# Kernel tuning notes

Measured on AMD Instinct MI355X. Metric: run time of the kernel, lower is better.

The kernel has to match this reference:

```python
import jax, jax.numpy as jnp
import numpy as np

# Qwen3.5 GatedDeltaNet dims
B, T, HID = 2, 2048, 2048
HK, HV, DK, DV, KW = 16, 32, 128, 128, 4   # k-heads, v-heads, head dims, conv kernel
R = HV // HK                                # GQA repeat factor = 2
KEY_DIM = HK * DK                           # 2048
VAL_DIM = HV * DV                           # 4096
CONV_DIM = 2 * KEY_DIM + VAL_DIM            # 8192
EPS = 1e-6


def setup_inputs() -> dict:
    key = jax.random.key(0)
    ks = jax.random.split(key, 10)
    w = lambda k, shape, s=0.02: (jax.random.normal(k, shape) * s).astype(jnp.float32)
    A = jax.random.uniform(ks[8], (HV,), minval=1e-3, maxval=16.0)
    return {
        "hidden_states": jax.random.normal(ks[0], (B, T, HID), jnp.float32),
        "W_qkv": w(ks[1], (HID, CONV_DIM)),
        "W_z": w(ks[2], (HID, VAL_DIM)),
        "W_b": w(ks[3], (HID, HV)),
        "W_a": w(ks[4], (HID, HV)),
        "conv_w": w(ks[5], (CONV_DIM, KW), 0.5),   # depthwise causal conv taps
        "dt_bias": jnp.ones((HV,), jnp.float32),
        "A_log": jnp.log(A).astype(jnp.float32),
        "norm_weight": jnp.ones((DV,), jnp.float32),
        "W_out": w(ks[9], (VAL_DIM, HID)),
    }


def _forward(hidden_states, W_qkv, W_z, W_b, W_a, conv_w, dt_bias, A_log, norm_weight, W_out):
    x = hidden_states
    # --- projections ---
    qkv = x @ W_qkv                                    # [B,T,CONV_DIM]
    z = x @ W_z                                        # [B,T,VAL_DIM]
    beta = jax.nn.sigmoid(x @ W_b)                     # [B,T,HV]
    alpha = x @ W_a                                    # [B,T,HV]
    g = -jnp.exp(A_log) * jax.nn.softplus(alpha + dt_bias)  # [B,T,HV] (log-decay <= 0)

    # --- fix_query_key_value_ordering: per-k-head interleaved layout ---
    qkv = qkv.reshape(B, T, HK, 2 * DK + R * DV)
    q, k, v = jnp.split(qkv, [DK, 2 * DK], axis=3)
    mixed = jnp.concatenate([q.reshape(B, T, -1), k.reshape(B, T, -1), v.reshape(B, T, -1)], axis=-1)

    # --- causal depthwise short conv (kernel 4) + SiLU ---
    xp = jnp.pad(mixed, ((0, 0), (KW - 1, 0), (0, 0)))
    conv = sum(conv_w[:, i] * xp[:, i:i + T, :] for i in range(KW))
    conv = jax.nn.silu(conv)

    q, k, v = jnp.split(conv, [KEY_DIM, 2 * KEY_DIM], axis=-1)
    q = q.reshape(B, T, HK, DK)
    k = k.reshape(B, T, HK, DK)
    v = v.reshape(B, T, HV, DV)
    gate = z.reshape(B, T, HV, DV)

    # GQA: repeat q,k heads to match v heads
    q = jnp.repeat(q, R, axis=2)                       # [B,T,HV,DK]
    k = jnp.repeat(k, R, axis=2)

    # l2-norm q,k (use_qk_l2norm_in_kernel=True) and default scale 1/sqrt(DK)
    q = q / jnp.sqrt(jnp.sum(q * q, axis=-1, keepdims=True) + 1e-6)
    k = k / jnp.sqrt(jnp.sum(k * k, axis=-1, keepdims=True) + 1e-6)
    q = q * (DK ** -0.5)

    # --- gated delta rule recurrence (scan over time) ---
    # state S: [B,HV,DK,DV];  S_t = a_t*S_{t-1} + k_t (beta_t*(v_t - (a_t*S_{t-1})^T k_t))^T
    def step(S, inp):
        qt, kt, vt, gt, bt = inp                       # [B,HV,DK],[B,HV,DK],[B,HV,DV],[B,HV],[B,HV]
        S = S * jnp.exp(gt)[:, :, None, None]
        kv = jnp.einsum('bhk,bhkv->bhv', kt, S)
        delta = bt[..., None] * (vt - kv)              # [B,HV,DV]
        S = S + kt[..., None] * delta[:, :, None, :]
        o = jnp.einsum('bhk,bhkv->bhv', qt, S)
        return S, o

    tfirst = lambda a: jnp.moveaxis(a, 1, 0)           # [T,B,...]
    S0 = jnp.zeros((B, HV, DK, DV), q.dtype)
    _, o = jax.lax.scan(step, S0, (tfirst(q), tfirst(k), tfirst(v), tfirst(g), tfirst(beta)))
    o = jnp.moveaxis(o, 0, 1)                          # [B,T,HV,DV]

    # --- gated RMSNorm: rmsnorm(o) * silu(gate) * weight ---
    var = jnp.mean(o * o, axis=-1, keepdims=True)
    o = o * jax.lax.rsqrt(var + EPS)
    o = o * jax.nn.silu(gate)
    o = o * norm_weight

    return o.reshape(B, T, VAL_DIM) @ W_out            # [B,T,HID]


def reference(hidden_states, W_qkv, W_z, W_b, W_a, conv_w, dt_bias, A_log, norm_weight, W_out):
    return _forward(hidden_states, W_qkv, W_z, W_b, W_a, conv_w, dt_bias, A_log, norm_weight, W_out)
```

## Files before the change

kernel.cpp:

```cpp
#include <hip/hip_runtime.h>


#define T_LEN 2048
#define MROWS 4096

typedef __bf16 bf16x8 __attribute__((ext_vector_type(8)));
typedef float f32x4 __attribute__((ext_vector_type(4)));

#define MFMA(a, b, c) __builtin_amdgcn_mfma_f32_16x16x32_bf16((a), (b), (c), 0, 0, 0)

__device__ __forceinline__ unsigned short f2bf(float f) {
  unsigned int u = __float_as_uint(f);
  unsigned int r = (u + 0x7fffu + ((u >> 16) & 1u)) >> 16;
  return (unsigned short)r;
}
__device__ __forceinline__ float bf2f(unsigned short u) {
  return __uint_as_float(((unsigned int)u) << 16);
}
__device__ __forceinline__ void gload_lds16(const void* g, void* l) {
  __builtin_amdgcn_global_load_lds(
      (const __attribute__((address_space(1))) unsigned int*)g,
      (__attribute__((address_space(3))) unsigned int*)l, 16, 0, 0);
}

__global__ __launch_bounds__(256) void f32_to_bf16_vec(const float* __restrict__ src,
                                                       unsigned short* __restrict__ dst,
                                                       int n4) {
  int i = blockIdx.x * 256 + threadIdx.x;
  if (i >= n4) return;
  float4 v = ((const float4*)src)[i];
  ushort4 o;
  o.x = f2bf(v.x); o.y = f2bf(v.y); o.z = f2bf(v.z); o.w = f2bf(v.w);
  ((ushort4*)dst)[i] = o;
}

__global__ __launch_bounds__(256) void transpose_f2b(const float* __restrict__ src,
                                                     unsigned short* __restrict__ dst,
                                                     int R, int C) {
  __shared__ float tile[32][33];
  int tx = threadIdx.x & 31, ty = threadIdx.x >> 5;
  int c0 = blockIdx.x * 32, r0 = blockIdx.y * 32;
  #pragma unroll
  for (int i = ty; i < 32; i += 8)
    tile[i][tx] = src[(size_t)(r0 + i) * C + c0 + tx];
  __syncthreads();
  #pragma unroll
  for (int i = ty; i < 32; i += 8)
    dst[(size_t)(c0 + i) * R + r0 + tx] = f2bf(tile[tx][i]);
}

template <int OUTBF>
__global__ __launch_bounds__(512, 2) void gemm8p(const unsigned short* __restrict__ A, int lda,
                                                 const unsigned short* __restrict__ Bt, int ldb,
                                                 void* __restrict__ Cv, int ldc,
                                                 int M, int N, int K) {
  __shared__ unsigned short lds[65536];

  const int mtiles = M >> 8;
  const int nwg = gridDim.x, orig = blockIdx.x;
  const int q = nwg >> 3, r = nwg & 7;
  const int xcd = orig & 7, idx = orig >> 3;
  const int swz = (xcd < r ? xcd * (q + 1) : r * (q + 1) + (xcd - r) * q) + idx;
  const int m0 = (swz % mtiles) * 256;
  const int n0 = (swz / mtiles) * 256;

  const int tid = threadIdx.x, lane = tid & 63, wv = tid >> 6;
  const int wm = wv >> 2, wn = wv & 3;
  const int l15 = lane & 15, l4 = lane >> 4;

  f32x4 acc[8][4];
  #pragma unroll
  for (int i = 0; i < 8; i++)
    #pragma unroll
    for (int j = 0; j < 4; j++) acc[i][j] = f32x4{0.f, 0.f, 0.f, 0.f};

  const int NT = K >> 6;

  auto SHALF = [&](int t, int op, int h) {
    unsigned short* base = lds + (t & 1) * 32768 + op * 16384 + h * 8192;
    const unsigned short* G = op ? Bt : A;
    const int ld = op ? ldb : lda;
    const int r0g = (op ? n0 : m0) + h * 128;
    const int k0 = t << 6;
    #pragma unroll
    for (int is = 0; is < 2; is++) {
      int ow = is * 8192 + wv * 1024;
      int o = ow + lane * 16;
      int row = o >> 7, colB = o & 127;
      int scol = colB ^ ((row & 7) << 4);
      gload_lds16(G + (size_t)(r0g + row) * ld + k0 + (scol >> 1), base + (ow >> 1));
    }
  };

  bf16x8 aF[4][2], bF[2][2];
  auto RD_A = [&](int t, int qm) {
    const unsigned short* base = lds + (t & 1) * 32768 + qm * 8192;
    #pragma unroll
    for (int mi = 0; mi < 4; mi++) {
      int ra = wm * 64 + mi * 16 + l15;
      int sw = (ra & 7) << 4;
      #pragma unroll
      for (int kh = 0; kh < 2; kh++) {
        int colB = kh * 64 + l4 * 16;
        aF[mi][kh] = *(const bf16x8*)(base + ra * 64 + ((colB ^ sw) >> 1));
      }
    }
  };
  auto RD_B = [&](int t, int qn) {
    const unsigned short* base = lds + (t & 1) * 32768 + 16384 + qn * 8192;
    #pragma unroll
    for (int ni = 0; ni < 2; ni++) {
      int rb = wn * 32 + ni * 16 + l15;
      int sw = (rb & 7) << 4;
      #pragma unroll
      for (int kh = 0; kh < 2; kh++) {
        int colB = kh * 64 + l4 * 16;
        bF[ni][kh] = *(const bf16x8*)(base + rb * 64 + ((colB ^ sw) >> 1));
      }
    }
  };
  auto COMPUTE = [&](int qm, int qn) {
    __builtin_amdgcn_s_setprio(1);
    #pragma unroll
    for (int mi = 0; mi < 4; mi++)
      #pragma unroll
      for (int ni = 0; ni < 2; ni++)
        #pragma unroll
        for (int kh = 0; kh < 2; kh++)
          acc[qm * 4 + mi][qn * 2 + ni] =
              MFMA(aF[mi][kh], bF[ni][kh], acc[qm * 4 + mi][qn * 2 + ni]);
    __builtin_amdgcn_s_setprio(0);
  };
  auto SBAR = [&]() {
    __builtin_amdgcn_sched_barrier(0);
    __builtin_amdgcn_s_barrier();
    __builtin_amdgcn_sched_barrier(0);
  };

  SHALF(0, 0, 0); SHALF(0, 1, 0); SHALF(0, 1, 1); SHALF(0, 0, 1);
  asm volatile("s_waitcnt vmcnt(4)" ::: "memory");
  SBAR();

  for (int t = 0; t < NT; t++) {
    const bool lastT = (t + 1 >= NT);
    RD_A(t, 0); RD_B(t, 0);
    if (!lastT) SHALF(t + 1, 0, 0);
    COMPUTE(0, 0);
    if (!lastT) asm volatile("s_waitcnt vmcnt(4)" ::: "memory");
    else        asm volatile("s_waitcnt vmcnt(2)" ::: "memory");
    SBAR();
    RD_B(t, 1);
    if (!lastT) SHALF(t + 1, 1, 0);
    COMPUTE(0, 1);
    if (!lastT) asm volatile("s_waitcnt vmcnt(4)" ::: "memory");
    else        asm volatile("s_waitcnt vmcnt(0)" ::: "memory");
    SBAR();
    RD_A(t, 1);
    if (!lastT) SHALF(t + 1, 1, 1);
    COMPUTE(1, 1);
    RD_B(t, 0);
    if (!lastT) SHALF(t + 1, 0, 1);
    COMPUTE(1, 0);
    if (!lastT) {
      asm volatile("s_waitcnt vmcnt(4)" ::: "memory");
      SBAR();
    }
  }

  #pragma unroll
  for (int i = 0; i < 8; i++) {
    int grow = m0 + (i >> 2) * 128 + wm * 64 + (i & 3) * 16 + l4 * 4;
    #pragma unroll
    for (int j = 0; j < 4; j++) {
      int gcol = n0 + (j >> 1) * 128 + wn * 32 + (j & 1) * 16 + l15;
      if (OUTBF) {
        unsigned short* cp = (unsigned short*)Cv + (size_t)grow * ldc + gcol;
        #pragma unroll
        for (int rr = 0; rr < 4; rr++) cp[(size_t)rr * ldc] = f2bf(acc[i][j][rr]);
      } else {
        float* cp = (float*)Cv + (size_t)grow * ldc + gcol;
        #pragma unroll
        for (int rr = 0; rr < 4; rr++) cp[(size_t)rr * ldc] = acc[i][j][rr];
      }
    }
  }
}

template <int OUTBF, int BN>
__global__ __launch_bounds__(512, 2) void gemm256(const unsigned short* __restrict__ A, int lda,
                                                  const unsigned short* __restrict__ Bt, int ldb,
                                                  void* __restrict__ Cv, int ldc,
                                                  int M, int N, int K) {
  constexpr int BUFSZ = 16384 + BN * 64;
  constexpr int BISS = BN / 64;
  constexpr int IS = 4 + BISS;
  constexpr int WMv = (BN == 256) ? 2 : 4;
  constexpr int MSUB = 256 / (WMv * 16);
  constexpr int MSPAN = 256 / WMv;

  __shared__ unsigned short lds[2 * BUFSZ];

  const int mtiles = M >> 8;
  const int nwg = gridDim.x;
  const int orig = blockIdx.x;
  const int q = nwg >> 3, r = nwg & 7;
  const int xcd = orig & 7, idx = orig >> 3;
  const int swz = (xcd < r ? xcd * (q + 1) : r * (q + 1) + (xcd - r) * q) + idx;
  const int m0 = (swz % mtiles) * 256;
  const int n0 = (swz / mtiles) * BN;

  const int tid = threadIdx.x, lane = tid & 63, wv = tid >> 6;
  const int wm = (BN == 256) ? (wv >> 2) : (wv >> 1);
  const int wn = (BN == 256) ? (wv & 3) : (wv & 1);
  const int l15 = lane & 15, l4 = lane >> 4;

  f32x4 acc[MSUB][4];
  #pragma unroll
  for (int i = 0; i < MSUB; i++)
    #pragma unroll
    for (int j = 0; j < 4; j++) acc[i][j] = f32x4{0.f, 0.f, 0.f, 0.f};

  const int NT = K >> 6;

  auto STAGE = [&](int kt) {
    unsigned short* base = lds + (kt & 1) * BUFSZ;
    const int k0 = kt << 6;
    #pragma unroll
    for (int is = 0; is < 4; is++) {
      int ow = is * 8192 + wv * 1024;
      int o = ow + lane * 16;
      int row = o >> 7, colB = o & 127;
      int scol = colB ^ ((row & 7) << 4);
      gload_lds16(A + (size_t)(m0 + row) * lda + k0 + (scol >> 1), base + (ow >> 1));
    }
    #pragma unroll
    for (int is = 0; is < BISS; is++) {
      int ow = is * 8192 + wv * 1024;
      int o = ow + lane * 16;
      int row = o >> 7, colB = o & 127;
      int scol = colB ^ ((row & 7) << 4);
      gload_lds16(Bt + (size_t)(n0 + row) * ldb + k0 + (scol >> 1), base + 16384 + (ow >> 1));
    }
  };

  STAGE(0);
  if (NT > 1) STAGE(1);
  if constexpr (IS == 8) asm volatile("s_waitcnt vmcnt(8)" ::: "memory");
  else                   asm volatile("s_waitcnt vmcnt(6)" ::: "memory");
  __builtin_amdgcn_sched_barrier(0);
  __builtin_amdgcn_s_barrier();
  __builtin_amdgcn_sched_barrier(0);

  for (int t = 0; t < NT; t++) {
    const unsigned short* Abuf = lds + (t & 1) * BUFSZ;
    const unsigned short* Bbuf = Abuf + 16384;
    bf16x8 bF[4][2];
    #pragma unroll
    for (int n = 0; n < 4; n++) {
      int rb = wn * 64 + n * 16 + l15;
      int sw = (rb & 7) << 4;
      #pragma unroll
      for (int ks = 0; ks < 2; ks++) {
        int colB = (ks * 32 + l4 * 8) * 2;
        bF[n][ks] = *(const bf16x8*)(Bbuf + rb * 64 + ((colB ^ sw) >> 1));
      }
    }
    __builtin_amdgcn_s_setprio(1);
    #pragma unroll
    for (int m = 0; m < MSUB; m++) {
      int ra = wm * MSPAN + m * 16 + l15;
      int sw = (ra & 7) << 4;
      int c0b = l4 * 16;
      bf16x8 a0 = *(const bf16x8*)(Abuf + ra * 64 + ((c0b ^ sw) >> 1));
      bf16x8 a1 = *(const bf16x8*)(Abuf + ra * 64 + (((64 + c0b) ^ sw) >> 1));
      #pragma unroll
      for (int n = 0; n < 4; n++) {
        acc[m][n] = MFMA(a0, bF[n][0], acc[m][n]);
        acc[m][n] = MFMA(a1, bF[n][1], acc[m][n]);
      }
    }
    __builtin_amdgcn_s_setprio(0);
    __builtin_amdgcn_sched_barrier(0);
    __builtin_amdgcn_s_barrier();
    __builtin_amdgcn_sched_barrier(0);
    if (t + 2 < NT) STAGE(t + 2);
    if (t + 1 < NT) {
      if (t + 2 < NT) {
        if constexpr (IS == 8) asm volatile("s_waitcnt vmcnt(8)" ::: "memory");
        else                   asm volatile("s_waitcnt vmcnt(6)" ::: "memory");
      } else {
        asm volatile("s_waitcnt vmcnt(0)" ::: "memory");
      }
      __builtin_amdgcn_sched_barrier(0);
      __builtin_amdgcn_s_barrier();
      __builtin_amdgcn_sched_barrier(0);
    }
  }

  #pragma unroll
  for (int m = 0; m < MSUB; m++) {
    int grow = m0 + wm * MSPAN + m * 16 + l4 * 4;
    #pragma unroll
    for (int n = 0; n < 4; n++) {
      int gcol = n0 + wn * 64 + n * 16 + l15;
      if (OUTBF) {
        unsigned short* cp = (unsigned short*)Cv + (size_t)grow * ldc + gcol;
        #pragma unroll
        for (int rr = 0; rr < 4; rr++) cp[(size_t)rr * ldc] = f2bf(acc[m][n][rr]);
      } else {
        float* cp = (float*)Cv + (size_t)grow * ldc + gcol;
        #pragma unroll
        for (int rr = 0; rr < 4; rr++) cp[(size_t)rr * ldc] = acc[m][n][rr];
      }
    }
  }
}

template <int OUTBF>
__global__ __launch_bounds__(256) void gemm_bf16(const unsigned short* __restrict__ A, int lda,
                                                 const unsigned short* __restrict__ Bt, int ldb,
                                                 void* __restrict__ Cv, int ldc,
                                                 int M, int N, int K) {
  __shared__ unsigned short As[128 * 64];
  __shared__ unsigned short Bs[128 * 64];
  const int tid = threadIdx.x, lane = tid & 63, wv = tid >> 6;
  const int wr = wv >> 1, wc = wv & 1;
  const int m0 = blockIdx.y * 128, n0 = blockIdx.x * 128;
  const int lrow8 = lane >> 3;
  const int lk8 = (lane & 7) * 8;

  f32x4 acc[4][4];
  #pragma unroll
  for (int i = 0; i < 4; i++)
    #pragma unroll
    for (int j = 0; j < 4; j++) acc[i][j] = f32x4{0.f, 0.f, 0.f, 0.f};

  for (int k0 = 0; k0 < K; k0 += 64) {
    #pragma unroll
    for (int j = 0; j < 4; ++j) {
      int chunk = j * 4 + wv;
      int r = chunk * 8 + lrow8;
      gload_lds16(A + (size_t)(m0 + r) * lda + k0 + lk8, (void*)(As + chunk * 512));
      gload_lds16(Bt + (size_t)(n0 + r) * ldb + k0 + lk8, (void*)(Bs + chunk * 512));
    }
    __syncthreads();
    #pragma unroll
    for (int half = 0; half < 2; ++half) {
      int ko = half * 32 + (lane >> 4) * 8;
      bf16x8 af[4], bfr[4];
      #pragma unroll
      for (int i = 0; i < 4; i++) {
        int ra = wr * 64 + i * 16 + (lane & 15);
        af[i] = *(const bf16x8*)(As + ra * 64 + ko);
        int rb = wc * 64 + i * 16 + (lane & 15);
        bfr[i] = *(const bf16x8*)(Bs + rb * 64 + ko);
      }
      #pragma unroll
      for (int i = 0; i < 4; i++)
        #pragma unroll
        for (int j = 0; j < 4; j++)
          acc[i][j] = MFMA(af[i], bfr[j], acc[i][j]);
    }
    __syncthreads();
  }
  int cr4 = (lane >> 4) * 4;
  int cc = lane & 15;
  #pragma unroll
  for (int i = 0; i < 4; i++) {
    int row = m0 + wr * 64 + i * 16 + cr4;
    #pragma unroll
    for (int j = 0; j < 4; j++) {
      int col = n0 + wc * 64 + j * 16 + cc;
      if (OUTBF) {
        unsigned short* cp = (unsigned short*)Cv + (size_t)row * ldc + col;
        #pragma unroll
        for (int r = 0; r < 4; r++) cp[(size_t)r * ldc] = f2bf(acc[i][j][r]);
      } else {
        float* cp = (float*)Cv + (size_t)row * ldc + col;
        #pragma unroll
        for (int r = 0; r < 4; r++) cp[(size_t)r * ldc] = acc[i][j][r];
      }
    }
  }
}

__global__ __launch_bounds__(256) void beta_g_kernel(const unsigned short* __restrict__ ba,
                                                     const float* __restrict__ A_log,
                                                     const float* __restrict__ dt_bias,
                                                     unsigned short* __restrict__ betab,
                                                     float* __restrict__ g) {
  int i = blockIdx.x * 256 + threadIdx.x;
  int row = i >> 5, hv = i & 31;
  float rb = bf2f(ba[(size_t)row * 128 + hv]);
  float ra = bf2f(ba[(size_t)row * 128 + 32 + hv]);
  betab[i] = f2bf(1.f / (1.f + expf(-rb)));
  float xg = ra + dt_bias[hv];
  float sp = (xg > 20.f) ? xg : log1pf(expf(xg));
  g[i] = -expf(A_log[hv]) * sp;
}

__global__ __launch_bounds__(256) void conv_kernel(const unsigned short* __restrict__ qkv,
                                                   const float* __restrict__ conv_w,
                                                   unsigned short* __restrict__ out) {
  const int seg = blockIdx.x, tt = blockIdx.y, b = blockIdx.z;
  const int tid = threadIdx.x;
  const int c0 = seg * 128;
  const bool isq = seg < 16;
  int scb;
  if (isq) scb = seg * 512;
  else if (seg < 32) scb = (seg - 16) * 512 + 128;
  else scb = ((seg - 32) >> 1) * 512 + 256 + ((seg - 32) & 1) * 128;

  __shared__ unsigned short raw[35][136];
  __shared__ float cw[4][132];

  for (int i = tid; i < 512; i += 256) {
    int cl = i >> 2, tap = i & 3;
    cw[tap][cl] = conv_w[(size_t)(c0 + cl) * 4 + tap];
  }
  const int t0 = tt * 32;
  for (int i = tid; i < 560; i += 256) {
    int row = i >> 4, col = (i & 15) * 8;
    int gt = t0 - 3 + row;
    uint4 v = make_uint4(0u, 0u, 0u, 0u);
    if (gt >= 0) v = *(const uint4*)(qkv + (size_t)(b * T_LEN + gt) * 8192 + scb + col);
    *(uint4*)(&raw[row][col]) = v;
  }
  __syncthreads();
  const int s = tid >> 3, dg = tid & 7;
  union RawU { uint4 v[2]; unsigned short h[16]; };
  RawU u[4];
  #pragma unroll
  for (int i = 0; i < 4; i++) {
    const uint4* p = (const uint4*)&raw[s + i][dg * 16];
    u[i].v[0] = p[0]; u[i].v[1] = p[1];
  }
  float vals[16]; float ss = 0.f;
  #pragma unroll
  for (int j = 0; j < 16; j++) {
    float a = 0.f;
    #pragma unroll
    for (int i = 0; i < 4; i++) a = fmaf(cw[i][dg * 16 + j], bf2f(u[i].h[j]), a);
    a = a / (1.f + expf(-a));
    vals[j] = a; ss += a * a;
  }
  if (seg < 32) {
    ss += __shfl_xor(ss, 1); ss += __shfl_xor(ss, 2); ss += __shfl_xor(ss, 4);
    float sc = rsqrtf(ss + 1e-6f);
    if (isq) sc *= 0.08838834764831845f;
    #pragma unroll
    for (int j = 0; j < 16; j++) vals[j] *= sc;
  }
  union { uint4 v[2]; unsigned short h[16]; } ov;
  #pragma unroll
  for (int j = 0; j < 16; j++) ov.h[j] = f2bf(vals[j]);
  unsigned short* op = out + (size_t)(b * T_LEN + t0 + s) * 8192 + c0 + dg * 16;
  *(uint4*)(op) = ov.v[0];
  *(uint4*)(op + 8) = ov.v[1];
}

__global__ __launch_bounds__(256) void prep_kernel(const unsigned short* __restrict__ conv,
                                                   const float* __restrict__ g,
                                                   const unsigned short* __restrict__ betab,
                                                   unsigned short* __restrict__ M1g,
                                                   unsigned short* __restrict__ M2g,
                                                   unsigned char* __restrict__ vecs) {
  const int c = blockIdx.x, bh = blockIdx.y;
  const int b = bh >> 5, hv = bh & 31, hk = hv >> 1;
  const int bhc = bh * 32 + c;
  const int tid = threadIdx.x, lane = tid & 63, wv = tid >> 6;
  const int r0 = b * T_LEN + c * 64;
  const int l15 = lane & 15, l4 = lane >> 4;

  __shared__ unsigned short Kb[128 * 72];
  __shared__ unsigned short QbX[64 * 136];
  __shared__ unsigned short Lbf[64 * 72];
  __shared__ unsigned short Pb[64 * 72];
  __shared__ unsigned short WT[3 * 16 * 40];
  __shared__ float Gs[64], SCs[64], BLs[64];

  unsigned short* Qb = QbX;
  unsigned short* XTb = QbX;
  unsigned short* Xdrow = QbX + 4608;

  if (wv == 0) {
    float gt = g[(size_t)(r0 + lane) * 32 + hv];
    #pragma unroll
    for (int d = 1; d < 64; d <<= 1) {
      float o = __shfl_up(gt, (unsigned)d, 64);
      if (lane >= d) gt += o;
    }
    float GC = __shfl(gt, 63, 64);
    float lam = expf(gt);
    float beta = bf2f(betab[(size_t)(r0 + lane) * 32 + hv]);
    Gs[lane] = gt;
    SCs[lane] = expf(GC - gt);
    BLs[lane] = beta;
    unsigned short* vb16 = (unsigned short*)(vecs + (size_t)bhc * 272);
    vb16[lane] = f2bf(beta * lam);
    vb16[64 + lane] = f2bf(lam);
    if (lane == 0) *(float*)(vecs + (size_t)bhc * 272 + 256) = expf(GC);
  }
  const unsigned short* Kg = conv + (size_t)r0 * 8192 + 2048 + hk * 128;
  const unsigned short* Qg = conv + (size_t)r0 * 8192 + hk * 128;
  for (int u = tid; u < 1024; u += 256) {
    int row = u >> 4, col = (u & 15) * 8;
    *(uint4*)(&Kb[row * 136 + col]) = *(const uint4*)(Kg + (size_t)row * 8192 + col);
    *(uint4*)(&Qb[row * 136 + col]) = *(const uint4*)(Qg + (size_t)row * 8192 + col);
  }
  __syncthreads();

  {
    f32x4 akk[4], aqk[4];
    #pragma unroll
    for (int st = 0; st < 4; st++) { akk[st] = f32x4{0,0,0,0}; aqk[st] = f32x4{0,0,0,0}; }
    int trow = wv * 16 + l15;
    int klo = l4 * 8;
    #pragma unroll
    for (int ks = 0; ks < 4; ks++) {
      int ko = ks * 32 + klo;
      bf16x8 ak = *(const bf16x8*)(&Kb[trow * 136 + ko]);
      bf16x8 aq = *(const bf16x8*)(&Qb[trow * 136 + ko]);
      #pragma unroll
      for (int st = 0; st < 4; st++) {
        bf16x8 bk = *(const bf16x8*)(&Kb[(st * 16 + l15) * 136 + ko]);
        akk[st] = MFMA(ak, bk, akk[st]);
        aqk[st] = MFMA(aq, bk, aqk[st]);
      }
    }
    int orow = wv * 16 + l4 * 4;
    int oc = l15;
    #pragma unroll
    for (int st = 0; st < 4; st++)
      #pragma unroll
      for (int r = 0; r < 4; r++) {
        int t = orow + r, ssv = st * 16 + oc;
        float e = expf(fminf(Gs[t] - Gs[ssv], 0.f));
        Lbf[t * 72 + ssv] = f2bf((ssv < t) ? BLs[t] * e * akk[st][r] : 0.f);
        Pb[t * 72 + ssv] = f2bf((ssv <= t) ? e * aqk[st][r] : 0.f);
      }
  }
  __syncthreads();

  unsigned short ktv[32];
  {
    int dk = tid >> 1, tb = (tid & 1) * 32;
    #pragma unroll
    for (int i = 0; i < 32; i++)
      ktv[i] = f2bf(bf2f(Kb[(tb + i) * 136 + dk]) * SCs[tb + i]);
    for (int u = tid; u < 896; u += 256) {
      *(uint4*)(&QbX[u * 8]) = make_uint4(0u, 0u, 0u, 0u);
    }
    for (int u = tid; u < 240; u += 256) {
      *(uint4*)(&WT[u * 8]) = make_uint4(0u, 0u, 0u, 0u);
    }
  }
  __syncthreads();

  {
    int dk = tid >> 1, tb = (tid & 1) * 32;
    #pragma unroll
    for (int i = 0; i < 32; i++) Kb[dk * 72 + tb + i] = ktv[i];
  }
  {
    const int w16 = wv * 16;
    const int cc = l15;
    float xr[16];
    #pragma unroll
    for (int t = 0; t < 16; t++) {
      float acc = (cc == t) ? 1.f : 0.f;
      union { uint4 v[2]; unsigned short h[16]; } rw;
      const uint4* p = (const uint4*)(&Lbf[(w16 + t) * 72 + w16]);
      rw.v[0] = p[0]; rw.v[1] = p[1];
      #pragma unroll
      for (int s = 0; s < 16; s++) {
        if (s < t) acc = fmaf(-bf2f(rw.h[s]), xr[s], acc);
      }
      xr[t] = acc;
    }
    if (lane < 16) {
      #pragma unroll
      for (int t = 0; t < 16; t++) {
        unsigned short v = f2bf(xr[t]);
        XTb[(w16 + cc) * 72 + w16 + t] = v;
        Xdrow[wv * 640 + t * 40 + cc] = v;
      }
    }
  }
  __syncthreads();

  if (wv < 3) {
    const int j = wv;
    for (int i = j + 1; i < 4; i++) {
      f32x4 w_ = f32x4{0.f, 0.f, 0.f, 0.f};
      #pragma unroll
      for (int ks = 0; ks < 2; ks++) {
        int so = ks * 32 + l4 * 8;
        bf16x8 af = *(const bf16x8*)(&Lbf[(i * 16 + l15) * 72 + so]);
        bf16x8 bfv = *(const bf16x8*)(&XTb[(j * 16 + l15) * 72 + so]);
        w_ = MFMA(af, bfv, w_);
      }
      #pragma unroll
      for (int r = 0; r < 4; r++)
        WT[j * 640 + l15 * 40 + l4 * 4 + r] = f2bf(-w_[r]);
      f32x4 xij = f32x4{0.f, 0.f, 0.f, 0.f};
      {
        bf16x8 af = *(const bf16x8*)(&Xdrow[i * 640 + l15 * 40 + l4 * 8]);
        bf16x8 bfv = *(const bf16x8*)(&WT[j * 640 + l15 * 40 + l4 * 8]);
        xij = MFMA(af, bfv, xij);
      }
      #pragma unroll
      for (int r = 0; r < 4; r++)
        XTb[(j * 16 + l15) * 72 + i * 16 + l4 * 4 + r] = f2bf(xij[r]);
    }
  }
  __syncthreads();

  for (int tt = wv * 12; tt < wv * 12 + 12; tt++) {
    f32x4 acc = f32x4{0, 0, 0, 0};
    const unsigned short* Abase;
    int mrow, jc;
    if (tt < 16) { mrow = (tt >> 2) * 16; jc = (tt & 3) * 16; Abase = Pb + mrow * 72; }
    else { int i2 = tt - 16; mrow = (i2 >> 2) * 16; jc = (i2 & 3) * 16; Abase = Kb + mrow * 72; }
    #pragma unroll
    for (int ks = 0; ks < 2; ks++) {
      int so = ks * 32 + l4 * 8;
      bf16x8 af = *(const bf16x8*)(Abase + l15 * 72 + so);
      bf16x8 bfv = *(const bf16x8*)(&XTb[(jc + l15) * 72 + so]);
      acc = MFMA(af, bfv, acc);
    }
    int ro = mrow + l4 * 4, co = jc + l15;
    if (tt < 16) {
      #pragma unroll
      for (int r = 0; r < 4; r++)
        M1g[(size_t)bhc * 4096 + (ro + r) * 64 + co] = f2bf(acc[r]);
    } else {
      #pragma unroll
      for (int r = 0; r < 4; r++)
        M2g[(size_t)bhc * 8192 + (ro + r) * 64 + co] = f2bf(acc[r]);
    }
  }
}

__global__ __launch_bounds__(256) void seq_kernel(unsigned short* __restrict__ conv,
                                                  const unsigned short* __restrict__ M1g,
                                                  const unsigned short* __restrict__ M2g,
                                                  const unsigned char* __restrict__ vecs,
                                                  const unsigned short* __restrict__ betab) {
  const int dvs = blockIdx.x, bh = blockIdx.y;
  const int b = bh >> 5, hv = bh & 31, hk = hv >> 1;
  const int dv0 = dvs * 16;
  const int tid = threadIdx.x, lane = tid & 63, wv = tid >> 6;

  __shared__ unsigned short Kb[64 * 136], Qb[64 * 136];
  __shared__ float Sf[128 * 20];
  __shared__ unsigned short S0T[16 * 136];
  __shared__ unsigned short rhsT[16 * 72];

  for (int i = tid; i < 128 * 20; i += 256) Sf[i] = 0.f;
  for (int i = tid; i < 16 * 136; i += 256) S0T[i] = 0;
  __syncthreads();

  const int l15 = lane & 15, l4 = lane >> 4;
  const int trt = wv * 16;

  for (int c = 0; c < 32; c++) {
    const int r0 = b * T_LEN + c * 64;
    const int bhc = bh * 32 + c;
    const unsigned char* vb = vecs + (size_t)bhc * 272;
    const unsigned short* vb16 = (const unsigned short*)vb;
    #pragma unroll
    for (int j = 0; j < 4; j++) {
      int u = j * 256 + tid;
      int row = u >> 4, col = (u & 15) * 8;
      uint4 kv = *(const uint4*)(conv + (size_t)(r0 + row) * 8192 + 2048 + hk * 128 + col);
      uint4 qv = *(const uint4*)(conv + (size_t)(r0 + row) * 8192 + hk * 128 + col);
      *(uint4*)(&Kb[row * 136 + col]) = kv;
      float lam = bf2f(vb16[64 + row]);
      union { uint4 u4; unsigned short h[8]; } qq; qq.u4 = qv;
      #pragma unroll
      for (int e = 0; e < 8; e++) qq.h[e] = f2bf(bf2f(qq.h[e]) * lam);
      *(uint4*)(&Qb[row * 136 + col]) = qq.u4;
    }
    __syncthreads();
    {
      f32x4 acc = f32x4{0, 0, 0, 0};
      #pragma unroll
      for (int ks = 0; ks < 4; ks++) {
        int ko = ks * 32 + l4 * 8;
        bf16x8 af = *(const bf16x8*)(&Kb[(trt + l15) * 136 + ko]);
        bf16x8 bfv = *(const bf16x8*)(&S0T[l15 * 136 + ko]);
        acc = MFMA(af, bfv, acc);
      }
      #pragma unroll
      for (int r = 0; r < 4; r++) {
        int tl = trt + l4 * 4 + r;
        int t = r0 + tl;
        float beta = bf2f(betab[(size_t)t * 32 + hv]);
        float bl = bf2f(vb16[tl]);
        float vv = bf2f(conv[(size_t)t * 8192 + 4096 + hv * 128 + dv0 + l15]);
        rhsT[l15 * 72 + tl] = f2bf(beta * vv - bl * acc[r]);
      }
    }
    __syncthreads();
    {
      f32x4 acc = f32x4{0, 0, 0, 0};
      const unsigned short* m1b = M1g + (size_t)bhc * 4096;
      #pragma unroll
      for (int ks = 0; ks < 2; ks++) {
        int so = ks * 32 + l4 * 8;
        union { uint4 u4; bf16x8 h; } af;
        af.u4 = *(const uint4*)(m1b + (trt + l15) * 64 + so);
        bf16x8 bfv = *(const bf16x8*)(&rhsT[l15 * 72 + so]);
        acc = MFMA(af.h, bfv, acc);
      }
      #pragma unroll
      for (int ks = 0; ks < 4; ks++) {
        int ko = ks * 32 + l4 * 8;
        bf16x8 af = *(const bf16x8*)(&Qb[(trt + l15) * 136 + ko]);
        bf16x8 bfv = *(const bf16x8*)(&S0T[l15 * 136 + ko]);
        acc = MFMA(af, bfv, acc);
      }
      #pragma unroll
      for (int r = 0; r < 4; r++) {
        int t = r0 + trt + l4 * 4 + r;
        conv[(size_t)t * 8192 + 4096 + hv * 128 + dv0 + l15] = f2bf(acc[r]);
      }
    }
    {
      float lamC = *(const float*)(vb + 256);
      f32x4 sacc[2];
      const unsigned short* m2b = M2g + (size_t)bhc * 8192;
      #pragma unroll
      for (int dkt = 0; dkt < 2; dkt++) {
        int dkb = (wv * 2 + dkt) * 16;
        f32x4 a;
        #pragma unroll
        for (int r = 0; r < 4; r++) a[r] = lamC * Sf[(dkb + l4 * 4 + r) * 20 + l15];
        #pragma unroll
        for (int ks = 0; ks < 2; ks++) {
          int so = ks * 32 + l4 * 8;
          union { uint4 u4; bf16x8 h; } af;
          af.u4 = *(const uint4*)(m2b + (dkb + l15) * 64 + so);
          bf16x8 bfv = *(const bf16x8*)(&rhsT[l15 * 72 + so]);
          a = MFMA(af.h, bfv, a);
        }
        sacc[dkt] = a;
      }
      __syncthreads();
      #pragma unroll
      for (int dkt = 0; dkt < 2; dkt++) {
        int dkb = (wv * 2 + dkt) * 16;
        #pragma unroll
        for (int r = 0; r < 4; r++) {
          int dk = dkb + l4 * 4 + r;
          Sf[dk * 20 + l15] = sacc[dkt][r];
          S0T[l15 * 136 + dk] = f2bf(sacc[dkt][r]);
        }
      }
    }
    __syncthreads();
  }
}

__global__ __launch_bounds__(256) void rmsgate_kernel(unsigned short* __restrict__ conv,
                                                      const unsigned short* __restrict__ zg,
                                                      const float* __restrict__ nw) {
  int wid = blockIdx.x * 4 + (threadIdx.x >> 6);
  int lane = threadIdx.x & 63;
  int row = wid >> 5, hv = wid & 31;
  unsigned short* op = conv + (size_t)row * 8192 + 4096 + hv * 128;
  float o0 = bf2f(op[lane]), o1 = bf2f(op[64 + lane]);
  float ss = o0 * o0 + o1 * o1;
  #pragma unroll
  for (int m = 1; m < 64; m <<= 1) ss += __shfl_xor(ss, m);
  float r = rsqrtf(ss * (1.f / 128.f) + 1e-6f);
  const unsigned short* zp = zg + (size_t)row * 4096 + hv * 128;
  float g0 = bf2f(zp[lane]), g1 = bf2f(zp[64 + lane]);
  g0 = g0 / (1.f + expf(-g0));
  g1 = g1 / (1.f + expf(-g1));
  op[lane] = f2bf(o0 * r * g0 * nw[lane]);
  op[64 + lane] = f2bf(o1 * r * g1 * nw[64 + lane]);
}

extern "C" void kernel_launch(void* const* d_in, const int* in_sizes, int n_in,
                              void* d_out, int out_size, void* d_ws, size_t ws_size,
                              hipStream_t stream) {
  (void)in_sizes; (void)n_in; (void)out_size;
  const float* x       = (const float*)d_in[0];
  const float* W_qkv   = (const float*)d_in[1];
  const float* W_z     = (const float*)d_in[2];
  const float* W_b     = (const float*)d_in[3];
  const float* W_a     = (const float*)d_in[4];
  const float* conv_w  = (const float*)d_in[5];
  const float* dt_bias = (const float*)d_in[6];
  const float* A_log   = (const float*)d_in[7];
  const float* nw      = (const float*)d_in[8];
  const float* W_out   = (const float*)d_in[9];
  float* out = (float*)d_out;

  const size_t NEED = 169115648ULL;
  if (ws_size < NEED) return;

  char* ws = (char*)d_ws;
  unsigned short* qkv_bf = (unsigned short*)(ws + 0);
  unsigned short* M1g    = (unsigned short*)(ws + 0);
  unsigned short* M2g    = (unsigned short*)(ws + 16777216);
  unsigned short* WoutT  = (unsigned short*)(ws + 0);
  unsigned short* zg     = (unsigned short*)(ws + 67108864);
  unsigned short* WzT    = (unsigned short*)(ws + 100663296);
  unsigned short* x_bf   = (unsigned short*)(ws + 100663296 + 16777216);
  unsigned short* WqkvT  = (unsigned short*)(ws + 100663296 + 33554432);
  unsigned short* WbaT   = (unsigned short*)(ws + 100663296 + 33554432);
  unsigned short* ba     = (unsigned short*)(ws + 100663296 + 34078720);
  unsigned short* convb  = (unsigned short*)(ws + 100663296);
  unsigned short* betab  = (unsigned short*)(ws + 167772160);
  float* gbuf            = (float*)(ws + 168034304);
  unsigned char* vecs    = (unsigned char*)(ws + 168558592);

  const int M = MROWS;

  f32_to_bf16_vec<<<(M * 2048 / 4) / 256, 256, 0, stream>>>(x, x_bf, M * 2048 / 4);
  transpose_f2b<<<dim3(8192 / 32, 2048 / 32), 256, 0, stream>>>(W_qkv, WqkvT, 2048, 8192);
  transpose_f2b<<<dim3(4096 / 32, 2048 / 32), 256, 0, stream>>>(W_z, WzT, 2048, 4096);

  gemm8p<1><<<512, 512, 0, stream>>>(x_bf, 2048, WqkvT, 2048, qkv_bf, 8192, M, 8192, 2048);

  transpose_f2b<<<dim3(1, 64), 256, 0, stream>>>(W_b, WbaT, 2048, 32);
  transpose_f2b<<<dim3(1, 64), 256, 0, stream>>>(W_a, WbaT + (size_t)32 * 2048, 2048, 32);

  gemm8p<1><<<256, 512, 0, stream>>>(x_bf, 2048, WzT, 2048, zg, 4096, M, 4096, 2048);
  gemm_bf16<1><<<dim3(1, M / 128), 256, 0, stream>>>(x_bf, 2048, WbaT, 2048, ba, 128, M, 128, 2048);

  beta_g_kernel<<<(M * 32) / 256, 256, 0, stream>>>(ba, A_log, dt_bias, betab, gbuf);

  conv_kernel<<<dim3(64, 64, 2), 256, 0, stream>>>(qkv_bf, conv_w, convb);

  prep_kernel<<<dim3(32, 64), 256, 0, stream>>>(convb, gbuf, betab, M1g, M2g, vecs);

  seq_kernel<<<dim3(8, 64), 256, 0, stream>>>(convb, M1g, M2g, vecs, betab);

  rmsgate_kernel<<<32768, 256, 0, stream>>>(convb, zg, nw);

  transpose_f2b<<<dim3(2048 / 32, 4096 / 32), 256, 0, stream>>>(W_out, WoutT, 4096, 2048);
  gemm256<0, 128><<<256, 512, 0, stream>>>(convb + 4096, 8192, WoutT, 4096, out, 2048, M, 2048, 4096);
}
```

Measured before the change: 636.7 us.

## Merge dv-split seq_kernel blocks into one 512-thread block per head with register state

The recurrent chunk kernel previously launched 8 blocks per (batch, v-head), each owning 16 dv columns and each reloading the same K/Q chunk tiles and M1 data. Now a single 512-thread block handles all 128 dv columns of a head. Each wave keeps its 16-row dk slice of the f32 state in registers instead of in shared memory, and the bf16 transposed state is written to LDS once per chunk. This removes the redundant loads and one barrier, but it cuts the grid from 512 to 64 blocks and gives each block more serial work per chunk, which risks underfilling the GPU.

```diff
diff --git a/kernel.cpp b/kernel.cpp
--- a/kernel.cpp
+++ b/kernel.cpp
@@ -642,27 +642,30 @@
   }
 }
 
-__global__ __launch_bounds__(256) void seq_kernel(unsigned short* __restrict__ conv,
+__global__ __launch_bounds__(512) void seq_kernel(unsigned short* __restrict__ conv,
                                                   const unsigned short* __restrict__ M1g,
                                                   const unsigned short* __restrict__ M2g,
                                                   const unsigned char* __restrict__ vecs,
                                                   const unsigned short* __restrict__ betab) {
-  const int dvs = blockIdx.x, bh = blockIdx.y;
+  const int bh = blockIdx.x;
   const int b = bh >> 5, hv = bh & 31, hk = hv >> 1;
-  const int dv0 = dvs * 16;
   const int tid = threadIdx.x, lane = tid & 63, wv = tid >> 6;
+  const int l15 = lane & 15, l4 = lane >> 4;
 
   __shared__ unsigned short Kb[64 * 136], Qb[64 * 136];
-  __shared__ float Sf[128 * 20];
-  __shared__ unsigned short S0T[16 * 136];
-  __shared__ unsigned short rhsT[16 * 72];
-
-  for (int i = tid; i < 128 * 20; i += 256) Sf[i] = 0.f;
-  for (int i = tid; i < 16 * 136; i += 256) S0T[i] = 0;
+  __shared__ unsigned short S0T[128 * 136];
+  __shared__ unsigned short rhsT[128 * 72];
+
+  f32x4 S[8];
+  #pragma unroll
+  for (int i = 0; i < 8; i++) S[i] = f32x4{0.f, 0.f, 0.f, 0.f};
+
+  for (int i = tid; i < 2176; i += 512) *(uint4*)(&S0T[i * 8]) = make_uint4(0u, 0u, 0u, 0u);
   __syncthreads();
 
-  const int l15 = lane & 15, l4 = lane >> 4;
-  const int trt = wv * 16;
+  const int trt = (wv >> 1) * 16;
+  const int dgb = (wv & 1) * 64;
+  const int dkb = wv * 16;
 
   for (int c = 0; c < 32; c++) {
     const int r0 = b * T_LEN + c * 64;
@@ -670,8 +673,8 @@
     const unsigned char* vb = vecs + (size_t)bhc * 272;
     const unsigned short* vb16 = (const unsigned short*)vb;
     #pragma unroll
-    for (int j = 0; j < 4; j++) {
-      int u = j * 256 + tid;
+    for (int j = 0; j < 2; j++) {
+      int u = j * 512 + tid;
       int row = u >> 4, col = (u & 15) * 8;
       uint4 kv = *(const uint4*)(conv + (size_t)(r0 + row) * 8192 + 2048 + hk * 128 + col);
       uint4 qv = *(const uint4*)(conv + (size_t)(r0 + row) * 8192 + hk * 128 + col);
@@ -683,13 +686,15 @@
       *(uint4*)(&Qb[row * 136 + col]) = qq.u4;
     }
     __syncthreads();
-    {
+    #pragma unroll
+    for (int dt = 0; dt < 4; dt++) {
+      int dv0 = dgb + dt * 16;
       f32x4 acc = f32x4{0, 0, 0, 0};
       #pragma unroll
       for (int ks = 0; ks < 4; ks++) {
         int ko = ks * 32 + l4 * 8;
         bf16x8 af = *(const bf16x8*)(&Kb[(trt + l15) * 136 + ko]);
-        bf16x8 bfv = *(const bf16x8*)(&S0T[l15 * 136 + ko]);
+        bf16x8 bfv = *(const bf16x8*)(&S0T[(dv0 + l15) * 136 + ko]);
         acc = MFMA(af, bfv, acc);
       }
       #pragma unroll
@@ -699,67 +704,60 @@
         float beta = bf2f(betab[(size_t)t * 32 + hv]);
         float bl = bf2f(vb16[tl]);
         float vv = bf2f(conv[(size_t)t * 8192 + 4096 + hv * 128 + dv0 + l15]);
-        rhsT[l15 * 72 + tl] = f2bf(beta * vv - bl * acc[r]);
+        rhsT[(dv0 + l15) * 72 + tl] = f2bf(beta * vv - bl * acc[r]);
       }
     }
     __syncthreads();
     {
-      f32x4 acc = f32x4{0, 0, 0, 0};
       const unsigned short* m1b = M1g + (size_t)bhc * 4096;
       #pragma unroll
-      for (int ks = 0; ks < 2; ks++) {
-        int so = ks * 32 + l4 * 8;
-        union { uint4 u4; bf16x8 h; } af;
-        af.u4 = *(const uint4*)(m1b + (trt + l15) * 64 + so);
-        bf16x8 bfv = *(const bf16x8*)(&rhsT[l15 * 72 + so]);
-        acc = MFMA(af.h, bfv, acc);
-      }
-      #pragma unroll
-      for (int ks = 0; ks < 4; ks++) {
-        int ko = ks * 32 + l4 * 8;
-        bf16x8 af = *(const bf16x8*)(&Qb[(trt + l15) * 136 + ko]);
-        bf16x8 bfv = *(const bf16x8*)(&S0T[l15 * 136 + ko]);
-        acc = MFMA(af, bfv, acc);
-      }
-      #pragma unroll
-      for (int r = 0; r < 4; r++) {
-        int t = r0 + trt + l4 * 4 + r;
-        conv[(size_t)t * 8192 + 4096 + hv * 128 + dv0 + l15] = f2bf(acc[r]);
-      }
-    }
-    {
+      for (int dt = 0; dt < 4; dt++) {
+        int dv0 = dgb + dt * 16;
+        f32x4 acc = f32x4{0, 0, 0, 0};
+        #pragma unroll
+        for (int ks = 0; ks < 2; ks++) {
+          int so = ks * 32 + l4 * 8;
+          union { uint4 u4; bf16x8 h; } af;
+          af.u4 = *(const uint4*)(m1b + (trt + l15) * 64 + so);
+          bf16x8 bfv = *(const bf16x8*)(&rhsT[(dv0 + l15) * 72 + so]);
+          acc = MFMA(af.h, bfv, acc);
+        }
+        #pragma unroll
+        for (int ks = 0; ks < 4; ks++) {
+          int ko = ks * 32 + l4 * 8;
+          bf16x8 af = *(const bf16x8*)(&Qb[(trt + l15) * 136 + ko]);
+          bf16x8 bfv = *(const bf16x8*)(&S0T[(dv0 + l15) * 136 + ko]);
+          acc = MFMA(af, bfv, acc);
+        }
+        #pragma unroll
+        for (int r = 0; r < 4; r++) {
+          int t = r0 + trt + l4 * 4 + r;
+          conv[(size_t)t * 8192 + 4096 + hv * 128 + dv0 + l15] = f2bf(acc[r]);
+        }
+      }
       float lamC = *(const float*)(vb + 256);
-      f32x4 sacc[2];
       const unsigned short* m2b = M2g + (size_t)bhc * 8192;
       #pragma unroll
-      for (int dkt = 0; dkt < 2; dkt++) {
-        int dkb = (wv * 2 + dkt) * 16;
-        f32x4 a;
-        #pragma unroll
-        for (int r = 0; r < 4; r++) a[r] = lamC * Sf[(dkb + l4 * 4 + r) * 20 + l15];
+      for (int dvt = 0; dvt < 8; dvt++) {
+        f32x4 a = S[dvt];
+        a[0] *= lamC; a[1] *= lamC; a[2] *= lamC; a[3] *= lamC;
         #pragma unroll
         for (int ks = 0; ks < 2; ks++) {
           int so = ks * 32 + l4 * 8;
           union { uint4 u4; bf16x8 h; } af;
           af.u4 = *(const uint4*)(m2b + (dkb + l15) * 64 + so);
-          bf16x8 bfv = *(const bf16x8*)(&rhsT[l15 * 72 + so]);
+          bf16x8 bfv = *(const bf16x8*)(&rhsT[(dvt * 16 + l15) * 72 + so]);
           a = MFMA(af.h, bfv, a);
         }
-        sacc[dkt] = a;
-      }
-      __syncthreads();
-      #pragma unroll
-      for (int dkt = 0; dkt < 2; dkt++) {
-        int dkb = (wv * 2 + dkt) * 16;
-        #pragma unroll
-        for (int r = 0; r < 4; r++) {
-          int dk = dkb + l4 * 4 + r;
-          Sf[dk * 20 + l15] = sacc[dkt][r];
-          S0T[l15 * 136 + dk] = f2bf(sacc[dkt][r]);
-        }
+        S[dvt] = a;
       }
     }
     __syncthreads();
+    #pragma unroll
+    for (int dvt = 0; dvt < 8; dvt++)
+      #pragma unroll
+      for (int r = 0; r < 4; r++)
+        S0T[(dvt * 16 + l15) * 136 + dkb + l4 * 4 + r] = f2bf(S[dvt][r]);
   }
 }
 
@@ -838,7 +836,7 @@
 
   prep_kernel<<<dim3(32, 64), 256, 0, stream>>>(convb, gbuf, betab, M1g, M2g, vecs);
 
-  seq_kernel<<<dim3(8, 64), 256, 0, stream>>>(convb, M1g, M2g, vecs, betab);
+  seq_kernel<<<64, 512, 0, stream>>>(convb, M1g, M2g, vecs, betab);
 
   rmsgate_kernel<<<32768, 256, 0, stream>>>(convb, zg, nw);
 
```

Measured after the change: 628.2 us. No clear change (-1.3%).
